# Kernel tuning notes

Hardware: AMD Instinct MI355X
Metric: run time of the kernel (lower is better)

## Reference

```python
import jax, jax.numpy as jnp
import numpy as np

N_NODES = 100000
N_EDGES = 1000000
D = 64
N_LAYERS = 3
LN_EPS = 1e-5


def setup_inputs() -> dict:
    key = jax.random.key(0)
    ks = jax.random.split(key, 12)
    s = 1.0 / np.sqrt(D)
    return {
        "feats": jax.random.normal(ks[0], (N_NODES, D), jnp.float32),
        "src": jax.random.randint(ks[1], (N_EDGES,), 0, N_NODES, jnp.int32),
        "dst": jax.random.randint(ks[2], (N_EDGES,), 0, N_NODES, jnp.int32),
        # GraphConv weights/biases (stacked over layers; in==hid==out==D)
        "conv_W": jax.random.normal(ks[3], (N_LAYERS, D, D), jnp.float32) * s,
        "conv_b": jnp.zeros((N_LAYERS, D), jnp.float32),
        # residual Linear per layer
        "res_W": jax.random.normal(ks[4], (N_LAYERS, D, D), jnp.float32) * s,
        "res_b": jnp.zeros((N_LAYERS, D), jnp.float32),
        # LayerNorm affine per layer
        "ln_g": jnp.ones((N_LAYERS, D), jnp.float32),
        "ln_b": jnp.zeros((N_LAYERS, D), jnp.float32),
        # final linear_prediction
        "pred_W": jax.random.normal(ks[5], (D, D), jnp.float32) * s,
        "pred_b": jnp.zeros((D,), jnp.float32),
    }


def _layer_norm(h, g, b):
    mu = jnp.mean(h, axis=-1, keepdims=True)
    var = jnp.mean(jnp.square(h - mu), axis=-1, keepdims=True)
    return (h - mu) * jax.lax.rsqrt(var + LN_EPS) * g + b


def reference(feats, src, dst, conv_W, conv_b, res_W, res_b, ln_g, ln_b, pred_W, pred_b):
    n = feats.shape[0]
    ones = jnp.ones(src.shape[0], feats.dtype)
    # DGL GraphConv norm='both', degrees clamped to >= 1
    out_deg = jnp.clip(jax.ops.segment_sum(ones, src, num_segments=n), 1.0, None)
    in_deg = jnp.clip(jax.ops.segment_sum(ones, dst, num_segments=n), 1.0, None)
    out_norm = jax.lax.rsqrt(out_deg)[:, None]  # [N,1]
    in_norm = jax.lax.rsqrt(in_deg)[:, None]

    h = feats
    h_final = jnp.zeros_like(feats)
    for i in range(N_LAYERS):
        # GraphConv: scale src, sum-aggregate over edges, scale dst, linear
        msg = (h * out_norm)[src]                                   # [E, D]
        agg = jax.ops.segment_sum(msg, dst, num_segments=n) * in_norm
        conv = agg @ conv_W[i] + conv_b[i]
        # residual linear + LayerNorm + relu (dropout p=0) + JK accumulate
        h = conv + h @ res_W[i] + res_b[i]
        h = jax.nn.relu(_layer_norm(h, ln_g[i], ln_b[i]))
        h_final = h_final + h
    return h_final @ pred_W + pred_b
```

## Files before the change

### kernel.cpp

```cpp
#include <hip/hip_runtime.h>
#include <hip/hip_bf16.h>

#define DD 64
#define NBLK 128
#define MAXBUK 1024
#define BSHIFT 7
#define NCTR 64

typedef __attribute__((ext_vector_type(8))) short short8v;
typedef __attribute__((ext_vector_type(4))) float f32x4;

__device__ __forceinline__ unsigned pk_bf16(float a, float b) {
    __hip_bfloat162 h = __float22bfloat162_rn(make_float2(a, b));
    unsigned u; __builtin_memcpy(&u, &h, 4); return u;
}
__device__ __forceinline__ short f2bf_s(float f) {
    union { float f; unsigned u; } x; x.f = f;
    unsigned r = x.u + 0x7fff + ((x.u >> 16) & 1);
    return (short)(r >> 16);
}
__device__ __forceinline__ float bf_lo(unsigned u) { return __int_as_float(u << 16); }
__device__ __forceinline__ float bf_hi(unsigned u) { return __int_as_float(u & 0xffff0000u); }
__device__ __forceinline__ short8v u4_to_s8(uint4 u) {
    union { uint4 u; short8v s; } x; x.u = u; return x.s;
}
__device__ __forceinline__ int ofs_at(const int* __restrict__ c,
                                      const int* __restrict__ bs, int i) {
    return c[i] + bs[i >> 8];
}


__global__ __launch_bounds__(256) void part_count(
        const int* __restrict__ src, const int* __restrict__ dst,
        int* __restrict__ cnt, int* __restrict__ wctr, int E, int nbuk, int ce,
        int chunk) {
    __shared__ int hd[MAXBUK], hs[MAXBUK];
    if (blockIdx.x == 0) {
        for (int i = threadIdx.x; i < 3 * NCTR; i += 256)
            wctr[i * 32] = (i & (NCTR - 1)) * chunk;
    }
    for (int i = threadIdx.x; i < MAXBUK; i += 256) { hd[i] = 0; hs[i] = 0; }
    __syncthreads();
    int e0 = blockIdx.x * ce;
    int e1 = min(e0 + ce, E);
    for (int e = e0 + (int)threadIdx.x; e < e1; e += 256) {
        atomicAdd(&hd[dst[e] >> BSHIFT], 1);
        atomicAdd(&hs[src[e] >> BSHIFT], 1);
    }
    __syncthreads();
    int L2 = nbuk * NBLK;
    for (int b = threadIdx.x; b < nbuk; b += 256) {
        cnt[b * NBLK + blockIdx.x]      = hd[b];
        cnt[L2 + b * NBLK + blockIdx.x] = hs[b];
    }
}

__global__ void scan1p(int* __restrict__ a, int* __restrict__ bsums, int L) {
    __shared__ int tmp[256];
    int gid = blockIdx.x * 256 + threadIdx.x;
    int v = (gid < L) ? a[gid] : 0;
    tmp[threadIdx.x] = v;
    __syncthreads();
    for (int off = 1; off < 256; off <<= 1) {
        int t = (threadIdx.x >= off) ? tmp[threadIdx.x - off] : 0;
        __syncthreads();
        tmp[threadIdx.x] += t;
        __syncthreads();
    }
    if (gid < L) a[gid] = tmp[threadIdx.x] - v;
    if (threadIdx.x == 255) bsums[blockIdx.x] = tmp[255];
}
__global__ void scan2p(int* __restrict__ bsums, int nb) {
    __shared__ int tmp[1024];
    int v = (threadIdx.x < (unsigned)nb) ? bsums[threadIdx.x] : 0;
    tmp[threadIdx.x] = v;
    __syncthreads();
    for (int off = 1; off < 1024; off <<= 1) {
        int t = (threadIdx.x >= off) ? tmp[threadIdx.x - off] : 0;
        __syncthreads();
        tmp[threadIdx.x] += t;
        __syncthreads();
    }
    if (threadIdx.x < (unsigned)nb) bsums[threadIdx.x] = tmp[threadIdx.x] - v;
}

__global__ __launch_bounds__(256) void part_scatter(
        const int* __restrict__ src, const int* __restrict__ dst,
        const int* __restrict__ cnt, const int* __restrict__ bsA,
        unsigned int* __restrict__ partD, unsigned char* __restrict__ partS,
        int E, int nbuk, int ce) {
    __shared__ int cd[MAXBUK], cs[MAXBUK];
    int L2 = nbuk * NBLK;
    for (int b = threadIdx.x; b < nbuk; b += 256) {
        cd[b] = ofs_at(cnt, bsA, b * NBLK + blockIdx.x);
        cs[b] = ofs_at(cnt, bsA, L2 + b * NBLK + blockIdx.x) - E;
    }
    __syncthreads();
    int e0 = blockIdx.x * ce;
    int e1 = min(e0 + ce, E);
    for (int e = e0 + (int)threadIdx.x; e < e1; e += 256) {
        int s = src[e], d = dst[e];
        int pd = atomicAdd(&cd[d >> BSHIFT], 1);
        partD[pd] = ((unsigned)(d & 127) << 17) | (unsigned)s;
        int ps = atomicAdd(&cs[s >> BSHIFT], 1);
        partS[ps] = (unsigned char)(s & 127);
    }
}

__global__ __launch_bounds__(256) void bucket_all(
        const unsigned int* __restrict__ partD, const unsigned char* __restrict__ partS,
        const int* __restrict__ cnt, const int* __restrict__ bsA,
        const float* __restrict__ feats,
        int* __restrict__ rowptr, int* __restrict__ esrc,
        float* __restrict__ inn, float* __restrict__ outn, float* __restrict__ rs,
        unsigned short* __restrict__ hsv,
        int E, int nbuk, int n) {
    __shared__ int hi[128], sc[128], cu[128], ho[128];
    __shared__ float son[128];
    int b = blockIdx.x, tid = threadIdx.x;
    int L2 = nbuk * NBLK;
    int e0 = ofs_at(cnt, bsA, b * NBLK);
    int e1 = (b + 1 < nbuk) ? ofs_at(cnt, bsA, (b + 1) * NBLK) : E;
    int f0 = ofs_at(cnt, bsA, L2 + b * NBLK) - E;
    int f1 = (b + 1 < nbuk) ? ofs_at(cnt, bsA, L2 + (b + 1) * NBLK) - E : E;
    if (tid < 128) { hi[tid] = 0; ho[tid] = 0; }
    __syncthreads();
    for (int e = e0 + tid; e < e1; e += 256) atomicAdd(&hi[partD[e] >> 17], 1);
    for (int e = f0 + tid; e < f1; e += 256) atomicAdd(&ho[(int)partS[e]], 1);
    __syncthreads();
    if (tid < 128) sc[tid] = hi[tid];
    __syncthreads();
    for (int off = 1; off < 128; off <<= 1) {
        int t = (tid < 128 && tid >= off) ? sc[tid - off] : 0;
        __syncthreads();
        if (tid < 128) sc[tid] += t;
        __syncthreads();
    }
    int nodeBase = b << BSHIFT;
    if (tid < 128) {
        int excl = e0 + sc[tid] - hi[tid];
        cu[tid] = excl;
        float oc = (float)max(ho[tid], 1);
        float on = rsqrtf(oc);
        son[tid] = on;
        int v = nodeBase + tid;
        if (v < n) {
            rowptr[v] = excl;
            inn[v] = rsqrtf((float)max(hi[tid], 1));
            outn[v] = on;
            rs[v]   = sqrtf(oc);
        }
    }
    if (b == 0 && tid == 0) rowptr[n] = E;
    __syncthreads();
    for (int e = e0 + tid; e < e1; e += 256) {
        unsigned u = partD[e];
        int p = atomicAdd(&cu[u >> 17], 1);
        esrc[p] = (int)(u & 0x1FFFFu);
    }
    for (int idx = tid; idx < 128 * 8; idx += 256) {
        int vl = idx >> 3, c = idx & 7;
        int v = nodeBase + vl;
        if (v < n) {
            float s = son[vl];
            const float4* fp = (const float4*)(feats + (size_t)v * DD) + c * 2;
            float4 g0 = fp[0], g1 = fp[1];
            uint4 o;
            o.x = pk_bf16(g0.x * s, g0.y * s); o.y = pk_bf16(g0.z * s, g0.w * s);
            o.z = pk_bf16(g1.x * s, g1.y * s); o.w = pk_bf16(g1.z * s, g1.w * s);
            *(uint4*)&hsv[(size_t)v * DD + c * 8] = o;
        }
    }
}

__global__ __launch_bounds__(256) void gcn_kernel(
    const int* __restrict__ rowptr, const int* __restrict__ esrc,
    const float* __restrict__ inn, const float* __restrict__ rs,
    const float* __restrict__ outn,
    const unsigned short* __restrict__ hs_in,
    const float* __restrict__ Wc, const float* __restrict__ bc,
    const float* __restrict__ Wr, const float* __restrict__ br,
    const float* __restrict__ Wp, const float* __restrict__ pb,
    const float* __restrict__ g, const float* __restrict__ bb,
    unsigned short* __restrict__ hs_out, float* __restrict__ h_final,
    float* __restrict__ pred_out, int* __restrict__ wctr, int chunk,
    int first, int last, int n)
{
    __shared__ __align__(16) short sWf[24 * 64 * 8];
    __shared__ __align__(16) short sXa[4][16 * 72];
    __shared__ float sEps[4 * 64];

    int lane = threadIdx.x & 63;
    int wave = threadIdx.x >> 6;
    int q   = lane & 15;
    int gg  = lane >> 4;
    int q8  = lane & 7;
    int o8  = lane >> 3;

    for (int idx = threadIdx.x; idx < 64; idx += blockDim.x) {
        sEps[idx]       = bc[idx] + br[idx];
        sEps[64 + idx]  = g[idx];
        sEps[128 + idx] = bb[idx];
        sEps[192 + idx] = pb[idx];
    }
    for (int f = wave * 6; f < wave * 6 + 6; ++f) {
        int mat = f >> 3, ft = (f >> 1) & 3, kc = f & 1;
        const float* Ws = (mat == 0) ? Wc : (mat == 1) ? Wr : Wp;
        int feat = ft * 16 + q;
        int k0 = kc * 32 + gg * 8;
        short8v fr;
        #pragma unroll
        for (int j = 0; j < 8; ++j) fr[j] = f2bf_s(Ws[(k0 + j) * DD + feat]);
        *(short8v*)&sWf[(f * 64 + lane) * 8] = fr;
    }
    __syncthreads();

    short* xrow_w = &sXa[wave][0];
    const short8v* wf = (const short8v*)sWf;
    int ngrp = (n + 15) >> 4;

    int c = blockIdx.x & (NCTR - 1);
    int* ctr = wctr + c * 32;
    int lim = min((c + 1) * chunk, ngrp);

    int grp = 0;
    if (lane == 0) grp = atomicAdd(ctr, 1);
    grp = __shfl(grp, 0);

    while (grp < lim) {
        int gnext = 0;
        if (lane == 0) gnext = atomicAdd(ctr, 1);

        int vbase = grp << 4;
        int vo = vbase + q;
        int vsel = min(vo, n - 1);

        const uint4* hrow = (const uint4*)(hs_in + (size_t)vsel * DD);
        uint4 bh0u = hrow[gg];
        uint4 bh1u = hrow[4 + gg];
        float rsv  = rs[vsel];
        float innv = inn[vsel];

        int rp = rowptr[min(vbase + min(lane, 16), n)];
        int stA = __shfl(rp, o8);     int dgA = __shfl(rp, o8 + 1) - stA;
        int stB = __shfl(rp, o8 + 8); int dgB = __shfl(rp, o8 + 9) - stB;

        #pragma unroll
        for (int hh = 0; hh < 2; ++hh) {
            int st = hh ? stB : stA;
            int dg = hh ? dgB : dgA;
            int mdg = dg;
            mdg = max(mdg, __shfl_xor(mdg, 8));
            mdg = max(mdg, __shfl_xor(mdg, 16));
            mdg = max(mdg, __shfl_xor(mdg, 32));

            float a[8];
            #pragma unroll
            for (int cc = 0; cc < 8; ++cc) a[cc] = 0.0f;

            int id0 = (0 < dg) ? esrc[st + 0] : 0;  float m0 = (0 < dg) ? 1.f : 0.f;
            int id1 = (1 < dg) ? esrc[st + 1] : 0;  float m1 = (1 < dg) ? 1.f : 0.f;
            int id2 = (2 < dg) ? esrc[st + 2] : 0;  float m2 = (2 < dg) ? 1.f : 0.f;
            int id3 = (3 < dg) ? esrc[st + 3] : 0;  float m3 = (3 < dg) ? 1.f : 0.f;

            for (int t = 0; t < mdg; t += 4) {
                uint4 r0 = *(const uint4*)(hs_in + (size_t)id0 * DD + q8 * 8);
                uint4 r1 = *(const uint4*)(hs_in + (size_t)id1 * DD + q8 * 8);
                uint4 r2 = *(const uint4*)(hs_in + (size_t)id2 * DD + q8 * 8);
                uint4 r3 = *(const uint4*)(hs_in + (size_t)id3 * DD + q8 * 8);
                float c0 = m0, c1 = m1, c2 = m2, c3 = m3;
                int t4 = t + 4;
                id0 = (t4 + 0 < dg) ? esrc[st + t4 + 0] : 0;  m0 = (t4 + 0 < dg) ? 1.f : 0.f;
                id1 = (t4 + 1 < dg) ? esrc[st + t4 + 1] : 0;  m1 = (t4 + 1 < dg) ? 1.f : 0.f;
                id2 = (t4 + 2 < dg) ? esrc[st + t4 + 2] : 0;  m2 = (t4 + 2 < dg) ? 1.f : 0.f;
                id3 = (t4 + 3 < dg) ? esrc[st + t4 + 3] : 0;  m3 = (t4 + 3 < dg) ? 1.f : 0.f;
                a[0] = fmaf(bf_lo(r0.x), c0, a[0]); a[1] = fmaf(bf_hi(r0.x), c0, a[1]);
                a[2] = fmaf(bf_lo(r0.y), c0, a[2]); a[3] = fmaf(bf_hi(r0.y), c0, a[3]);
                a[4] = fmaf(bf_lo(r0.z), c0, a[4]); a[5] = fmaf(bf_hi(r0.z), c0, a[5]);
                a[6] = fmaf(bf_lo(r0.w), c0, a[6]); a[7] = fmaf(bf_hi(r0.w), c0, a[7]);
                a[0] = fmaf(bf_lo(r1.x), c1, a[0]); a[1] = fmaf(bf_hi(r1.x), c1, a[1]);
                a[2] = fmaf(bf_lo(r1.y), c1, a[2]); a[3] = fmaf(bf_hi(r1.y), c1, a[3]);
                a[4] = fmaf(bf_lo(r1.z), c1, a[4]); a[5] = fmaf(bf_hi(r1.z), c1, a[5]);
                a[6] = fmaf(bf_lo(r1.w), c1, a[6]); a[7] = fmaf(bf_hi(r1.w), c1, a[7]);
                a[0] = fmaf(bf_lo(r2.x), c2, a[0]); a[1] = fmaf(bf_hi(r2.x), c2, a[1]);
                a[2] = fmaf(bf_lo(r2.y), c2, a[2]); a[3] = fmaf(bf_hi(r2.y), c2, a[3]);
                a[4] = fmaf(bf_lo(r2.z), c2, a[4]); a[5] = fmaf(bf_hi(r2.z), c2, a[5]);
                a[6] = fmaf(bf_lo(r2.w), c2, a[6]); a[7] = fmaf(bf_hi(r2.w), c2, a[7]);
                a[0] = fmaf(bf_lo(r3.x), c3, a[0]); a[1] = fmaf(bf_hi(r3.x), c3, a[1]);
                a[2] = fmaf(bf_lo(r3.y), c3, a[2]); a[3] = fmaf(bf_hi(r3.y), c3, a[3]);
                a[4] = fmaf(bf_lo(r3.z), c3, a[4]); a[5] = fmaf(bf_hi(r3.z), c3, a[5]);
                a[6] = fmaf(bf_lo(r3.w), c3, a[6]); a[7] = fmaf(bf_hi(r3.w), c3, a[7]);
            }

            uint4 w4;
            w4.x = pk_bf16(a[0], a[1]); w4.y = pk_bf16(a[2], a[3]);
            w4.z = pk_bf16(a[4], a[5]); w4.w = pk_bf16(a[6], a[7]);
            *(uint4*)&xrow_w[(hh * 8 + o8) * 72 + q8 * 8] = w4;
        }

        const short* xr = &xrow_w[q * 72];
        short8v ba0 = *(const short8v*)&xr[gg * 8];
        short8v ba1 = *(const short8v*)&xr[32 + gg * 8];
        short8v sh0 = u4_to_s8(bh0u);
        short8v sh1 = u4_to_s8(bh1u);

        f32x4 accC[4], accR[4];
        #pragma unroll
        for (int ft = 0; ft < 4; ++ft) {
            f32x4 cq = {0.f, 0.f, 0.f, 0.f};
            cq = __builtin_amdgcn_mfma_f32_16x16x32_bf16(wf[(ft * 2 + 0) * 64 + lane], ba0, cq, 0, 0, 0);
            cq = __builtin_amdgcn_mfma_f32_16x16x32_bf16(wf[(ft * 2 + 1) * 64 + lane], ba1, cq, 0, 0, 0);
            accC[ft] = cq;
            f32x4 r = {0.f, 0.f, 0.f, 0.f};
            r = __builtin_amdgcn_mfma_f32_16x16x32_bf16(wf[(8 + ft * 2 + 0) * 64 + lane], sh0, r, 0, 0, 0);
            r = __builtin_amdgcn_mfma_f32_16x16x32_bf16(wf[(8 + ft * 2 + 1) * 64 + lane], sh1, r, 0, 0, 0);
            accR[ft] = r;
        }

        f32x4 ac[4];
        #pragma unroll
        for (int ft = 0; ft < 4; ++ft) {
            float4 b4 = *(const float4*)&sEps[ft * 16 + gg * 4];
            ac[ft][0] = fmaf(innv, accC[ft][0], fmaf(rsv, accR[ft][0], b4.x));
            ac[ft][1] = fmaf(innv, accC[ft][1], fmaf(rsv, accR[ft][1], b4.y));
            ac[ft][2] = fmaf(innv, accC[ft][2], fmaf(rsv, accR[ft][2], b4.z));
            ac[ft][3] = fmaf(innv, accC[ft][3], fmaf(rsv, accR[ft][3], b4.w));
        }
        float s = 0.f;
        #pragma unroll
        for (int ft = 0; ft < 4; ++ft) s += ac[ft][0] + ac[ft][1] + ac[ft][2] + ac[ft][3];
        s += __shfl_xor(s, 16); s += __shfl_xor(s, 32);
        float mu = s * (1.0f / 64.0f);
        float vsum = 0.f;
        #pragma unroll
        for (int ft = 0; ft < 4; ++ft) {
            #pragma unroll
            for (int r = 0; r < 4; ++r) { float d = ac[ft][r] - mu; vsum += d * d; }
        }
        vsum += __shfl_xor(vsum, 16); vsum += __shfl_xor(vsum, 32);
        float rinv = rsqrtf(vsum * (1.0f / 64.0f) + 1e-5f);

        float4 yv[4];
        #pragma unroll
        for (int ft = 0; ft < 4; ++ft) {
            float4 g4 = *(const float4*)&sEps[64 + ft * 16 + gg * 4];
            float4 c4 = *(const float4*)&sEps[128 + ft * 16 + gg * 4];
            yv[ft].x = fmaxf((ac[ft][0] - mu) * rinv * g4.x + c4.x, 0.f);
            yv[ft].y = fmaxf((ac[ft][1] - mu) * rinv * g4.y + c4.y, 0.f);
            yv[ft].z = fmaxf((ac[ft][2] - mu) * rinv * g4.z + c4.z, 0.f);
            yv[ft].w = fmaxf((ac[ft][3] - mu) * rinv * g4.w + c4.w, 0.f);
        }

        if (!last) {
            if (vo < n) {
                float on = outn[vo];
                #pragma unroll
                for (int ft = 0; ft < 4; ++ft) {
                    size_t off = (size_t)vo * DD + ft * 16 + gg * 4;
                    uint2 p;
                    p.x = pk_bf16(yv[ft].x * on, yv[ft].y * on);
                    p.y = pk_bf16(yv[ft].z * on, yv[ft].w * on);
                    *(uint2*)&hs_out[off] = p;
                    if (first) {
                        *(float4*)&h_final[off] = yv[ft];
                    } else {
                        float4 hf = *(const float4*)&h_final[off];
                        hf.x += yv[ft].x; hf.y += yv[ft].y;
                        hf.z += yv[ft].z; hf.w += yv[ft].w;
                        *(float4*)&h_final[off] = hf;
                    }
                }
            }
        } else {
            #pragma unroll
            for (int ft = 0; ft < 4; ++ft) {
                float4 hf = make_float4(0.f, 0.f, 0.f, 0.f);
                if (vo < n) {
                    float4 old = *(const float4*)&h_final[(size_t)vo * DD + ft * 16 + gg * 4];
                    hf.x = old.x + yv[ft].x; hf.y = old.y + yv[ft].y;
                    hf.z = old.z + yv[ft].z; hf.w = old.w + yv[ft].w;
                }
                uint2 p;
                p.x = pk_bf16(hf.x, hf.y);
                p.y = pk_bf16(hf.z, hf.w);
                *(uint2*)&xrow_w[q * 72 + ft * 16 + gg * 4] = p;
            }
            short8v bp0 = *(const short8v*)&xr[gg * 8];
            short8v bp1 = *(const short8v*)&xr[32 + gg * 8];
            #pragma unroll
            for (int ft = 0; ft < 4; ++ft) {
                f32x4 p = {0.f, 0.f, 0.f, 0.f};
                p = __builtin_amdgcn_mfma_f32_16x16x32_bf16(wf[(16 + ft * 2 + 0) * 64 + lane], bp0, p, 0, 0, 0);
                p = __builtin_amdgcn_mfma_f32_16x16x32_bf16(wf[(16 + ft * 2 + 1) * 64 + lane], bp1, p, 0, 0, 0);
                if (vo < n) {
                    float4 b4 = *(const float4*)&sEps[192 + ft * 16 + gg * 4];
                    float4 o = make_float4(p[0] + b4.x, p[1] + b4.y, p[2] + b4.z, p[3] + b4.w);
                    *(float4*)&pred_out[(size_t)vo * DD + ft * 16 + gg * 4] = o;
                }
            }
        }

        grp = __shfl(gnext, 0);
    }
}

extern "C" void kernel_launch(void* const* d_in, const int* in_sizes, int n_in,
                              void* d_out, int out_size, void* d_ws, size_t ws_size,
                              hipStream_t stream) {
    const float* feats  = (const float*)d_in[0];
    const int*   src    = (const int*)d_in[1];
    const int*   dst    = (const int*)d_in[2];
    const float* conv_W = (const float*)d_in[3];
    const float* conv_b = (const float*)d_in[4];
    const float* res_W  = (const float*)d_in[5];
    const float* res_b  = (const float*)d_in[6];
    const float* ln_g   = (const float*)d_in[7];
    const float* ln_b   = (const float*)d_in[8];
    const float* pred_W = (const float*)d_in[9];
    const float* pred_b = (const float*)d_in[10];

    int N = in_sizes[0] / DD;
    int E = in_sizes[1];

    int nbuk = (N + (1 << BSHIFT) - 1) >> BSHIFT;
    int ce   = (E + NBLK - 1) / NBLK;
    int L    = nbuk * NBLK * 2;
    int nb   = (L + 255) / 256;
    int ngrp = (N + 15) >> 4;
    int chunk = (ngrp + NCTR - 1) / NCTR;

    int*   rowptr = (int*)d_ws;
    int*   cnt    = rowptr + (N + 1);
    int*   bsA    = cnt + MAXBUK * NBLK * 2;
    int*   wctr   = bsA + 1024;
    int*   esrc   = wctr + 3 * NCTR * 32;
    float* outn   = (float*)(esrc + E);
    float* inn    = outn + N;
    float* rs     = inn + N;
    float* base   = (float*)(((uintptr_t)(rs + N) + 15) & ~(uintptr_t)15);
    unsigned short* hsA = (unsigned short*)base;
    unsigned short* hsB = (unsigned short*)(base + (size_t)N * 32);
    float* hfin  = base + (size_t)N * 64;
    unsigned int*  partD = (unsigned int*)hfin;
    unsigned char* partS = (unsigned char*)(partD + E);

    part_count  <<<NBLK, 256, 0, stream>>>(src, dst, cnt, wctr, E, nbuk, ce, chunk);
    scan1p      <<<nb, 256, 0, stream>>>(cnt, bsA, L);
    scan2p      <<<1, 1024, 0, stream>>>(bsA, nb);
    part_scatter<<<NBLK, 256, 0, stream>>>(src, dst, cnt, bsA, partD, partS, E, nbuk, ce);
    bucket_all  <<<nbuk, 256, 0, stream>>>(partD, partS, cnt, bsA, feats, rowptr, esrc,
                                           inn, outn, rs, hsA, E, nbuk, N);

    const unsigned short* ins[3]  = {hsA, hsB, hsA};
    unsigned short*       outs[3] = {hsB, hsA, hsB};
    for (int l = 0; l < 3; ++l) {
        gcn_kernel<<<1024, 256, 0, stream>>>(
            rowptr, esrc, inn, rs, outn, ins[l],
            conv_W + (size_t)l * DD * DD, conv_b + (size_t)l * DD,
            res_W  + (size_t)l * DD * DD, res_b  + (size_t)l * DD,
            pred_W, pred_b,
            ln_g   + (size_t)l * DD,      ln_b   + (size_t)l * DD,
            outs[l], hfin, (float*)d_out, wctr + l * NCTR * 32, chunk,
            (l == 0) ? 1 : 0, (l == 2) ? 1 : 0, N);
    }
}
```

Measured before the change: 291.2 us.

## Fold block-sum scan into consumers and double partition block count

Removes the separate single-block scan2p launch. Each block of part_scatter and bucket_all now redundantly scans the block sums in shared memory before use. NBLK is doubled to 256, giving more blocks for the count and scatter passes and a larger count array (nb grows to about 1564 block sums). The intent is to cut one kernel launch and improve parallelism in partitioning, at the cost of redundant per-block scan work, including in each of the 782 bucket_all blocks.

```diff
diff --git a/kernel.cpp b/kernel.cpp
--- a/kernel.cpp
+++ b/kernel.cpp
@@ -2,7 +2,7 @@
 #include <hip/hip_bf16.h>
 
 #define DD 64
-#define NBLK 128
+#define NBLK 256
 #define MAXBUK 1024
 #define BSHIFT 7
 #define NCTR 64
@@ -24,11 +24,37 @@
 __device__ __forceinline__ short8v u4_to_s8(uint4 u) {
     union { uint4 u; short8v s; } x; x.u = u; return x.s;
 }
-__device__ __forceinline__ int ofs_at(const int* __restrict__ c,
-                                      const int* __restrict__ bs, int i) {
-    return c[i] + bs[i >> 8];
-}
-
+
+
+__device__ void scan_bs(const int* __restrict__ bsums, int nb,
+                        int* __restrict__ sbs, int* __restrict__ part) {
+    int tid = threadIdx.x;
+    int k = (nb + 255) >> 8;
+    int base = tid * k;
+    int s = 0;
+    for (int j = 0; j < k; ++j) {
+        int i = base + j;
+        int v = (i < nb) ? bsums[i] : 0;
+        sbs[i] = v;
+        s += v;
+    }
+    part[tid] = s;
+    __syncthreads();
+    for (int off = 1; off < 256; off <<= 1) {
+        int t = (tid >= off) ? part[tid - off] : 0;
+        __syncthreads();
+        part[tid] += t;
+        __syncthreads();
+    }
+    int run = part[tid] - s;
+    for (int j = 0; j < k; ++j) {
+        int i = base + j;
+        int v = sbs[i];
+        sbs[i] = run;
+        run += v;
+    }
+    __syncthreads();
+}
 
 __global__ __launch_bounds__(256) void part_count(
         const int* __restrict__ src, const int* __restrict__ dst,
@@ -70,30 +96,21 @@
     if (gid < L) a[gid] = tmp[threadIdx.x] - v;
     if (threadIdx.x == 255) bsums[blockIdx.x] = tmp[255];
 }
-__global__ void scan2p(int* __restrict__ bsums, int nb) {
-    __shared__ int tmp[1024];
-    int v = (threadIdx.x < (unsigned)nb) ? bsums[threadIdx.x] : 0;
-    tmp[threadIdx.x] = v;
-    __syncthreads();
-    for (int off = 1; off < 1024; off <<= 1) {
-        int t = (threadIdx.x >= off) ? tmp[threadIdx.x - off] : 0;
-        __syncthreads();
-        tmp[threadIdx.x] += t;
-        __syncthreads();
-    }
-    if (threadIdx.x < (unsigned)nb) bsums[threadIdx.x] = tmp[threadIdx.x] - v;
-}
 
 __global__ __launch_bounds__(256) void part_scatter(
         const int* __restrict__ src, const int* __restrict__ dst,
-        const int* __restrict__ cnt, const int* __restrict__ bsA,
+        const int* __restrict__ cnt, const int* __restrict__ bsums,
         unsigned int* __restrict__ partD, unsigned char* __restrict__ partS,
-        int E, int nbuk, int ce) {
+        int E, int nbuk, int ce, int nb) {
     __shared__ int cd[MAXBUK], cs[MAXBUK];
+    __shared__ int sbs[2048], part[256];
+    scan_bs(bsums, nb, sbs, part);
     int L2 = nbuk * NBLK;
     for (int b = threadIdx.x; b < nbuk; b += 256) {
-        cd[b] = ofs_at(cnt, bsA, b * NBLK + blockIdx.x);
-        cs[b] = ofs_at(cnt, bsA, L2 + b * NBLK + blockIdx.x) - E;
+        int i0 = b * NBLK + blockIdx.x;
+        int i1 = L2 + b * NBLK + blockIdx.x;
+        cd[b] = cnt[i0] + sbs[i0 >> 8];
+        cs[b] = cnt[i1] + sbs[i1 >> 8] - E;
     }
     __syncthreads();
     int e0 = blockIdx.x * ce;
@@ -109,20 +126,23 @@
 
 __global__ __launch_bounds__(256) void bucket_all(
         const unsigned int* __restrict__ partD, const unsigned char* __restrict__ partS,
-        const int* __restrict__ cnt, const int* __restrict__ bsA,
+        const int* __restrict__ cnt, const int* __restrict__ bsums,
         const float* __restrict__ feats,
         int* __restrict__ rowptr, int* __restrict__ esrc,
         float* __restrict__ inn, float* __restrict__ outn, float* __restrict__ rs,
         unsigned short* __restrict__ hsv,
-        int E, int nbuk, int n) {
+        int E, int nbuk, int n, int nb) {
     __shared__ int hi[128], sc[128], cu[128], ho[128];
     __shared__ float son[128];
+    __shared__ int sbs[2048], part[256];
+    scan_bs(bsums, nb, sbs, part);
     int b = blockIdx.x, tid = threadIdx.x;
     int L2 = nbuk * NBLK;
-    int e0 = ofs_at(cnt, bsA, b * NBLK);
-    int e1 = (b + 1 < nbuk) ? ofs_at(cnt, bsA, (b + 1) * NBLK) : E;
-    int f0 = ofs_at(cnt, bsA, L2 + b * NBLK) - E;
-    int f1 = (b + 1 < nbuk) ? ofs_at(cnt, bsA, L2 + (b + 1) * NBLK) - E : E;
+    int i0 = b * NBLK, i1 = (b + 1) * NBLK;
+    int e0 = cnt[i0] + sbs[i0 >> 8];
+    int e1 = (b + 1 < nbuk) ? (cnt[i1] + sbs[i1 >> 8]) : E;
+    int f0 = cnt[L2 + i0] + sbs[(L2 + i0) >> 8] - E;
+    int f1 = (b + 1 < nbuk) ? (cnt[L2 + i1] + sbs[(L2 + i1) >> 8] - E) : E;
     if (tid < 128) { hi[tid] = 0; ho[tid] = 0; }
     __syncthreads();
     for (int e = e0 + tid; e < e1; e += 256) atomicAdd(&hi[partD[e] >> 17], 1);
@@ -432,7 +452,7 @@
     int*   rowptr = (int*)d_ws;
     int*   cnt    = rowptr + (N + 1);
     int*   bsA    = cnt + MAXBUK * NBLK * 2;
-    int*   wctr   = bsA + 1024;
+    int*   wctr   = bsA + 2048;
     int*   esrc   = wctr + 3 * NCTR * 32;
     float* outn   = (float*)(esrc + E);
     float* inn    = outn + N;
@@ -446,10 +466,9 @@
 
     part_count  <<<NBLK, 256, 0, stream>>>(src, dst, cnt, wctr, E, nbuk, ce, chunk);
     scan1p      <<<nb, 256, 0, stream>>>(cnt, bsA, L);
-    scan2p      <<<1, 1024, 0, stream>>>(bsA, nb);
-    part_scatter<<<NBLK, 256, 0, stream>>>(src, dst, cnt, bsA, partD, partS, E, nbuk, ce);
+    part_scatter<<<NBLK, 256, 0, stream>>>(src, dst, cnt, bsA, partD, partS, E, nbuk, ce, nb);
     bucket_all  <<<nbuk, 256, 0, stream>>>(partD, partS, cnt, bsA, feats, rowptr, esrc,
-                                           inn, outn, rs, hsA, E, nbuk, N);
+                                           inn, outn, rs, hsA, E, nbuk, N, nb);
 
     const unsigned short* ins[3]  = {hsA, hsB, hsA};
     unsigned short*       outs[3] = {hsB, hsA, hsB};
```

After: 285.5 us, median of 2. About the same (-2.0%).
